# Kernel tuning notes

Hardware: AMD Instinct MI355X
Metric: run time of the kernel (lower is better)

Reference implementation:

```python
import jax, jax.numpy as jnp
import numpy as np

N, C, EMB_ROWS = 524288, 128, 32
SLOPE = 0.2  # leaky_relu negative slope


def setup_inputs() -> dict:
    key = jax.random.key(0)
    k1, k2, k3, k4, k5 = jax.random.split(key, 5)
    x = jax.random.normal(k1, (N, C), jnp.float32)
    perm = jax.random.permutation(k2, N)  # fixed stand-in for torch.randperm
    depth = jax.random.normal(k3, (EMB_ROWS, 128), jnp.float32)  # Embedding(32,128), N(0,1) init
    fan_in = 2 * C * 2
    bound = 1.0 / np.sqrt(fan_in)
    W = jax.random.uniform(k4, (C, 2 * C, 2), jnp.float32, -bound, bound)  # Conv1d weight (O,I,K)
    b = jax.random.uniform(k5, (C,), jnp.float32, -bound, bound)
    return {"x": x, "depth": depth, "W": W, "b": b, "perm": perm}


def reference(x, depth, W, b, perm):
    c = W.shape[0]
    x = x[perm]                      # random shuffle of rows
    x = x.T.reshape(1, c, -1)        # [1, C, N]
    i = 0
    # Python while over STATIC shapes -> unrolled at trace time (~log2(N) steps)
    while x.shape[-1] > 1:
        L = x.shape[-1]
        e = jnp.broadcast_to(depth[i].reshape(1, 128, 1), (1, 128, L))
        x = jnp.concatenate([x, e], axis=1)   # [1, 2C, L]
        x = jax.lax.conv_general_dilated(
            x, W, window_strides=(1,), padding="VALID",
            dimension_numbers=("NCH", "OIH", "NCH"))  # [1, C, L-1]
        x = x + b.reshape(1, -1, 1)
        x = jnp.where(x >= 0, x, SLOPE * x)   # leaky_relu(0.2)
        if x.shape[-1] == 1:
            break
        # MaxPool1d(2,2): floor(L/2), drops trailing element for odd L
        x = jax.lax.reduce_window(
            x, -jnp.inf, jax.lax.max,
            window_dimensions=(1, 1, 2), window_strides=(1, 1, 2),
            padding="VALID")
        i += 1
    return x.reshape(c, 1).T  # [1, C]
```

## Files before the change

kernel.cpp:

```cpp
#include <hip/hip_runtime.h>
#include <hip/hip_bf16.h>


typedef __bf16 v8bf __attribute__((ext_vector_type(8)));
typedef float v16f __attribute__((ext_vector_type(16)));

__device__ __forceinline__ ushort f2bf(float f) {
    __hip_bfloat16 h = __float2bfloat16(f);
    return *reinterpret_cast<ushort*>(&h);
}
__device__ __forceinline__ unsigned pack2(float lo, float hi) {
    return (unsigned)f2bf(lo) | ((unsigned)f2bf(hi) << 16);
}
__device__ __forceinline__ float leaky(float y) { return (y >= 0.f) ? y : 0.2f * y; }

#define ZACC {0.f,0.f,0.f,0.f,0.f,0.f,0.f,0.f,0.f,0.f,0.f,0.f,0.f,0.f,0.f,0.f}

__global__ void bias_kernel(const float* __restrict__ W, const float* __restrict__ b,
                            const float* __restrict__ depth, float* __restrict__ Bst) {
    int i = blockIdx.x, o = threadIdx.x;
    const float* Wo = W + (size_t)o * 512 + 256;
    const float* di = depth + (size_t)i * 128;
    float s = b[o];
#pragma unroll 8
    for (int c = 0; c < 128; ++c) s += di[c] * (Wo[2 * c] + Wo[2 * c + 1]);
    Bst[i * 128 + o] = s;
}

__global__ void repack_kernel(const float* __restrict__ W, ushort* __restrict__ A) {
    int o = blockIdx.x, c = threadIdx.x;
    float v = (c < 128) ? W[(size_t)o * 512 + 2 * c] : W[(size_t)o * 512 + 2 * (c - 128) + 1];
    A[o * 256 + c] = f2bf(v);
}

#define WAVE_SETUP()                                                          \
    const int tid = threadIdx.x;                                              \
    const int lane = tid & 63;                                                \
    const int w = tid >> 6;                                                   \
    const int n31 = lane & 31;                                                \
    const int h = lane >> 5;                                                  \
    v8bf af[16];                                                              \
    {                                                                         \
        const ushort* Arow = A + (size_t)(w * 32 + n31) * 256 + h * 8;        \
        _Pragma("unroll")                                                     \
        for (int s = 0; s < 16; ++s) af[s] = *(const v8bf*)&Arow[s * 16];     \
    }

#define LOAD_BIAS(dst_, Bs)                                                   \
    float dst_[16];                                                           \
    _Pragma("unroll")                                                         \
    for (int r = 0; r < 16; ++r)                                              \
        dst_[r] = (Bs)[w * 32 + (r & 3) + 8 * (r >> 2) + 4 * h];

#define MFMA_TILE_LDS(buf, r0_, r1_, acc)                                     \
    {                                                                         \
        const ushort* sp0 = (buf) + (r0_) * 128;                              \
        const ushort* sp1 = (buf) + (r1_) * 128;                              \
        const int mm0 = (r0_) & 15, mm1 = (r1_) & 15;                         \
        _Pragma("unroll")                                                     \
        for (int s = 0; s < 8; ++s)                                           \
            acc = __builtin_amdgcn_mfma_f32_32x32x16_bf16(                    \
                af[s], *(const v8bf*)&sp0[((2 * s + h) ^ mm0) * 8], acc, 0, 0, 0); \
        _Pragma("unroll")                                                     \
        for (int s = 0; s < 8; ++s)                                           \
            acc = __builtin_amdgcn_mfma_f32_32x32x16_bf16(                    \
                af[8 + s], *(const v8bf*)&sp1[((2 * s + h) ^ mm1) * 8], acc, 0, 0, 0); \
    }

__global__ __launch_bounds__(256)
void pair_fused(const ushort* __restrict__ Xin,
                const float* __restrict__ x0,
                const int* __restrict__ perm,
                const ushort* __restrict__ A,
                const float* __restrict__ Bst2,
                ushort* __restrict__ Y,
                int Lin, int Lp2, int stage0) {
    __shared__ __align__(16) ushort xin[132 * 128];
    __shared__ __align__(16) ushort mid[65 * 128];
    __shared__ int prow[132];

    const int U = blockIdx.x * 32;
    const int t0 = U * 4;

    if (stage0) {
        for (int r = threadIdx.x; r < 132; r += 256)
            prow[r] = perm[min(t0 + r, Lin - 1)];
        __syncthreads();
    }
    for (int idx = threadIdx.x; idx < 132 * 16; idx += 256) {
        int row = idx >> 4, ck = idx & 15;
        int t = min(t0 + row, Lin - 1);
        int dst = row * 128 + ((ck ^ (row & 15)) * 8);
        if (stage0) {
            const float* s = x0 + (size_t)prow[row] * 128 + ck * 8;
            float4 a = *(const float4*)s;
            float4 bq = *(const float4*)(s + 4);
            uint4 v;
            v.x = pack2(a.x, a.y);  v.y = pack2(a.z, a.w);
            v.z = pack2(bq.x, bq.y); v.w = pack2(bq.z, bq.w);
            *(uint4*)&xin[dst] = v;
        } else {
            *(uint4*)&xin[dst] = *(const uint4*)&Xin[(size_t)t * 128 + ck * 8];
        }
    }
    __syncthreads();

    WAVE_SETUP();

    {
        LOAD_BIAS(bias_r, Bst2);
#pragma unroll
        for (int ti = 0; ti < 5; ++ti) {
            const int p = 32 * ti + n31;
            const int r0 = min(p, 131), r1 = min(p + 1, 131);
            v16f acc = ZACC;
            MFMA_TILE_LDS(xin, r0, r1, acc);
            const int u1 = 16 * ti + (n31 >> 1);
            const bool act = !(lane & 1) && (u1 < 65);
#pragma unroll
            for (int q = 0; q < 4; ++q) {
                float pv[4];
#pragma unroll
                for (int j = 0; j < 4; ++j) {
                    float y = leaky(acc[4 * q + j] + bias_r[4 * q + j]);
                    float y2 = __shfl_xor(y, 1, 64);
                    pv[j] = fmaxf(y, y2);
                }
                if (act) {
                    uint2 v;
                    v.x = pack2(pv[0], pv[1]);
                    v.y = pack2(pv[2], pv[3]);
                    *(uint2*)&mid[u1 * 128 + (((4 * w + q) ^ (u1 & 15)) * 8) + 4 * h] = v;
                }
            }
        }
    }
    __syncthreads();

    {
        LOAD_BIAS(bias_r, Bst2 + 128);
#pragma unroll
        for (int ti = 0; ti < 2; ++ti) {
            const int p = 32 * ti + n31;
            v16f acc = ZACC;
            MFMA_TILE_LDS(mid, p, p + 1, acc);
            const int u2 = U + 16 * ti + (n31 >> 1);
            const bool act = !(lane & 1) && (u2 < Lp2);
#pragma unroll
            for (int q = 0; q < 4; ++q) {
                float pv[4];
#pragma unroll
                for (int j = 0; j < 4; ++j) {
                    float y = leaky(acc[4 * q + j] + bias_r[4 * q + j]);
                    float y2 = __shfl_xor(y, 1, 64);
                    pv[j] = fmaxf(y, y2);
                }
                if (act) {
                    uint2 v;
                    v.x = pack2(pv[0], pv[1]);
                    v.y = pack2(pv[2], pv[3]);
                    *(uint2*)&Y[(size_t)u2 * 128 + w * 32 + 8 * q + 4 * h] = v;
                }
            }
        }
    }
}

__global__ __launch_bounds__(256)
void tail_fused(const ushort* __restrict__ Xg, const ushort* __restrict__ A,
                const float* __restrict__ BstAll, float* __restrict__ out) {
    extern __shared__ __align__(16) ushort tbuf[];
    ushort* buf0 = tbuf;
    ushort* buf1 = tbuf + 255 * 128;

    WAVE_SETUP();

    int Lin = 511;
    for (int st = 0; st < 8; ++st) {
        const int Lp = (Lin - 1) >> 1;
        LOAD_BIAS(bias_r, BstAll + (size_t)(10 + st) * 128);
        ushort* dst = (st & 1) ? buf1 : buf0;
        const ushort* src = (st & 1) ? buf0 : buf1;
        const int ntiles = (Lin - 1 + 31) >> 5;
        for (int ti = 0; ti < ntiles; ++ti) {
            const int t = ti * 32 + n31;
            const int r0 = min(t, Lin - 1), r1 = min(t + 1, Lin - 1);
            v16f acc = ZACC;
            if (st == 0) {
                const ushort* p0 = Xg + (size_t)r0 * 128 + h * 8;
                const ushort* p1 = Xg + (size_t)r1 * 128 + h * 8;
#pragma unroll
                for (int s = 0; s < 8; ++s)
                    acc = __builtin_amdgcn_mfma_f32_32x32x16_bf16(
                        af[s], *(const v8bf*)&p0[s * 16], acc, 0, 0, 0);
#pragma unroll
                for (int s = 0; s < 8; ++s)
                    acc = __builtin_amdgcn_mfma_f32_32x32x16_bf16(
                        af[8 + s], *(const v8bf*)&p1[s * 16], acc, 0, 0, 0);
            } else {
                MFMA_TILE_LDS(src, r0, r1, acc);
            }
            const int u = t >> 1;
            const bool act = !(lane & 1) && (u < Lp);
#pragma unroll
            for (int q = 0; q < 4; ++q) {
                float pv[4];
#pragma unroll
                for (int j = 0; j < 4; ++j) {
                    float y = leaky(acc[4 * q + j] + bias_r[4 * q + j]);
                    float y2 = __shfl_xor(y, 1, 64);
                    pv[j] = fmaxf(y, y2);
                }
                if (act) {
                    if (st < 7) {
                        uint2 v;
                        v.x = pack2(pv[0], pv[1]);
                        v.y = pack2(pv[2], pv[3]);
                        *(uint2*)&dst[u * 128 + (((4 * w + q) ^ (u & 15)) * 8) + 4 * h] = v;
                    } else {
                        float4 o = {pv[0], pv[1], pv[2], pv[3]};
                        *(float4*)&out[w * 32 + 8 * q + 4 * h] = o;
                    }
                }
            }
        }
        __syncthreads();
        Lin = Lp;
    }
}

extern "C" void kernel_launch(void* const* d_in, const int* in_sizes, int n_in,
                              void* d_out, int out_size, void* d_ws, size_t ws_size,
                              hipStream_t stream) {
    const float* x     = (const float*)d_in[0];
    const float* depth = (const float*)d_in[1];
    const float* W     = (const float*)d_in[2];
    const float* b     = (const float*)d_in[3];
    const int*   perm  = (const int*)d_in[4];
    float* out = (float*)d_out;

    char* ws = (char*)d_ws;
    float*  Bst = (float*)ws;
    ushort* A   = (ushort*)(ws + 16384);
    ushort* R0  = (ushort*)(ws + 16384 + 65536);
    ushort* R1  = (ushort*)(ws + 16384 + 65536 + (size_t)131071 * 256);

    bias_kernel<<<18, 128, 0, stream>>>(W, b, depth, Bst);
    repack_kernel<<<128, 256, 0, stream>>>(W, A);

    pair_fused<<<4096, 256, 0, stream>>>(nullptr, x, perm, A, Bst, R0,
                                         524288, 131071, 1);
    pair_fused<<<1024, 256, 0, stream>>>(R0, nullptr, nullptr, A, Bst + 2 * 128, R1,
                                         131071, 32767, 0);
    pair_fused<<<256, 256, 0, stream>>>(R1, nullptr, nullptr, A, Bst + 4 * 128, R0,
                                        32767, 8191, 0);
    pair_fused<<<64, 256, 0, stream>>>(R0, nullptr, nullptr, A, Bst + 6 * 128, R1,
                                       8191, 2047, 0);
    pair_fused<<<16, 256, 0, stream>>>(R1, nullptr, nullptr, A, Bst + 8 * 128, R0,
                                       2047, 511, 0);
    tail_fused<<<1, 256, (255 + 127) * 128 * 2, stream>>>(R0, A, Bst, out);
}
```

Baseline: 555.9 us.

## Fuse all stages into one persistent cooperative kernel with grid syncs

Replaces the chain of seven launches (prep, five pair stages, tail) with a single cooperative persistent kernel that loops blocks over the tiles of each stage and separates stages with grid.sync, keeping the weight fragments in registers across stages. The tail now ping-pongs through global scratch instead of LDS, and the perm lookup is done per element instead of staged in shared memory. This is meant to remove launch gaps and tail-effect idle time between the small late stages. In exchange it adds grid-barrier cost and occupancy limits from cooperative launch, and the tail's global-memory round trips may be slower than LDS.

Measured after the change: 889.6 us. 60.0% more time.

```diff
diff --git a/kernel.cpp b/kernel.cpp
--- a/kernel.cpp
+++ b/kernel.cpp
@@ -1,5 +1,8 @@
 #include <hip/hip_runtime.h>
 #include <hip/hip_bf16.h>
+#include <hip/hip_cooperative_groups.h>
+
+namespace cg = cooperative_groups;
 
 
 typedef __bf16 v8bf __attribute__((ext_vector_type(8)));
@@ -16,83 +19,33 @@
 
 #define ZACC {0.f,0.f,0.f,0.f,0.f,0.f,0.f,0.f,0.f,0.f,0.f,0.f,0.f,0.f,0.f,0.f}
 
-__global__ void bias_kernel(const float* __restrict__ W, const float* __restrict__ b,
-                            const float* __restrict__ depth, float* __restrict__ Bst) {
-    int i = blockIdx.x, o = threadIdx.x;
-    const float* Wo = W + (size_t)o * 512 + 256;
-    const float* di = depth + (size_t)i * 128;
-    float s = b[o];
-#pragma unroll 8
-    for (int c = 0; c < 128; ++c) s += di[c] * (Wo[2 * c] + Wo[2 * c + 1]);
-    Bst[i * 128 + o] = s;
-}
-
-__global__ void repack_kernel(const float* __restrict__ W, ushort* __restrict__ A) {
-    int o = blockIdx.x, c = threadIdx.x;
-    float v = (c < 128) ? W[(size_t)o * 512 + 2 * c] : W[(size_t)o * 512 + 2 * (c - 128) + 1];
-    A[o * 256 + c] = f2bf(v);
-}
-
-#define WAVE_SETUP()                                                          \
-    const int tid = threadIdx.x;                                              \
-    const int lane = tid & 63;                                                \
-    const int w = tid >> 6;                                                   \
-    const int n31 = lane & 31;                                                \
-    const int h = lane >> 5;                                                  \
-    v8bf af[16];                                                              \
-    {                                                                         \
-        const ushort* Arow = A + (size_t)(w * 32 + n31) * 256 + h * 8;        \
-        _Pragma("unroll")                                                     \
-        for (int s = 0; s < 16; ++s) af[s] = *(const v8bf*)&Arow[s * 16];     \
-    }
-
-#define LOAD_BIAS(dst_, Bs)                                                   \
-    float dst_[16];                                                           \
-    _Pragma("unroll")                                                         \
-    for (int r = 0; r < 16; ++r)                                              \
-        dst_[r] = (Bs)[w * 32 + (r & 3) + 8 * (r >> 2) + 4 * h];
-
-#define MFMA_TILE_LDS(buf, r0_, r1_, acc)                                     \
-    {                                                                         \
-        const ushort* sp0 = (buf) + (r0_) * 128;                              \
-        const ushort* sp1 = (buf) + (r1_) * 128;                              \
-        const int mm0 = (r0_) & 15, mm1 = (r1_) & 15;                         \
-        _Pragma("unroll")                                                     \
-        for (int s = 0; s < 8; ++s)                                           \
-            acc = __builtin_amdgcn_mfma_f32_32x32x16_bf16(                    \
-                af[s], *(const v8bf*)&sp0[((2 * s + h) ^ mm0) * 8], acc, 0, 0, 0); \
-        _Pragma("unroll")                                                     \
-        for (int s = 0; s < 8; ++s)                                           \
-            acc = __builtin_amdgcn_mfma_f32_32x32x16_bf16(                    \
-                af[8 + s], *(const v8bf*)&sp1[((2 * s + h) ^ mm1) * 8], acc, 0, 0, 0); \
-    }
-
-__global__ __launch_bounds__(256)
-void pair_fused(const ushort* __restrict__ Xin,
-                const float* __restrict__ x0,
-                const int* __restrict__ perm,
-                const ushort* __restrict__ A,
-                const float* __restrict__ Bst2,
-                ushort* __restrict__ Y,
-                int Lin, int Lp2, int stage0) {
-    __shared__ __align__(16) ushort xin[132 * 128];
-    __shared__ __align__(16) ushort mid[65 * 128];
-    __shared__ int prow[132];
-
-    const int U = blockIdx.x * 32;
+__device__ __forceinline__ void load_af(const ushort* __restrict__ A, v8bf* af) {
+    const int lane = threadIdx.x & 63;
+    const int w = threadIdx.x >> 6;
+    const ushort* Arow = A + (size_t)(w * 32 + (lane & 31)) * 256 + (lane >> 5) * 8;
+#pragma unroll
+    for (int s = 0; s < 16; ++s) af[s] = *(const v8bf*)&Arow[s * 16];
+}
+
+__device__ void do_pair(int U, const ushort* __restrict__ Xin,
+                        const float* __restrict__ x0, const int* __restrict__ perm,
+                        const v8bf* af, const float* __restrict__ Bst2,
+                        ushort* __restrict__ Y, int Lin, int Lp2, int stage0,
+                        ushort* xin, ushort* mid) {
+    const int tid = threadIdx.x;
+    const int lane = tid & 63;
+    const int w = tid >> 6;
+    const int n31 = lane & 31;
+    const int h = lane >> 5;
     const int t0 = U * 4;
 
-    if (stage0) {
-        for (int r = threadIdx.x; r < 132; r += 256)
-            prow[r] = perm[min(t0 + r, Lin - 1)];
-        __syncthreads();
-    }
-    for (int idx = threadIdx.x; idx < 132 * 16; idx += 256) {
+    for (int idx = tid; idx < 132 * 16; idx += 256) {
         int row = idx >> 4, ck = idx & 15;
         int t = min(t0 + row, Lin - 1);
         int dst = row * 128 + ((ck ^ (row & 15)) * 8);
         if (stage0) {
-            const float* s = x0 + (size_t)prow[row] * 128 + ck * 8;
+            int pr = perm[t];
+            const float* s = x0 + (size_t)pr * 128 + ck * 8;
             float4 a = *(const float4*)s;
             float4 bq = *(const float4*)(s + 4);
             uint4 v;
@@ -105,16 +58,27 @@
     }
     __syncthreads();
 
-    WAVE_SETUP();
-
     {
-        LOAD_BIAS(bias_r, Bst2);
+        float bias_r[16];
+#pragma unroll
+        for (int r = 0; r < 16; ++r)
+            bias_r[r] = Bst2[w * 32 + (r & 3) + 8 * (r >> 2) + 4 * h];
 #pragma unroll
         for (int ti = 0; ti < 5; ++ti) {
             const int p = 32 * ti + n31;
             const int r0 = min(p, 131), r1 = min(p + 1, 131);
+            const ushort* sp0 = xin + r0 * 128;
+            const ushort* sp1 = xin + r1 * 128;
+            const int m0 = r0 & 15, m1 = r1 & 15;
             v16f acc = ZACC;
-            MFMA_TILE_LDS(xin, r0, r1, acc);
+#pragma unroll
+            for (int s = 0; s < 8; ++s)
+                acc = __builtin_amdgcn_mfma_f32_32x32x16_bf16(
+                    af[s], *(const v8bf*)&sp0[((2 * s + h) ^ m0) * 8], acc, 0, 0, 0);
+#pragma unroll
+            for (int s = 0; s < 8; ++s)
+                acc = __builtin_amdgcn_mfma_f32_32x32x16_bf16(
+                    af[8 + s], *(const v8bf*)&sp1[((2 * s + h) ^ m1) * 8], acc, 0, 0, 0);
             const int u1 = 16 * ti + (n31 >> 1);
             const bool act = !(lane & 1) && (u1 < 65);
 #pragma unroll
@@ -138,12 +102,25 @@
     __syncthreads();
 
     {
-        LOAD_BIAS(bias_r, Bst2 + 128);
+        float bias_r[16];
+#pragma unroll
+        for (int r = 0; r < 16; ++r)
+            bias_r[r] = Bst2[128 + w * 32 + (r & 3) + 8 * (r >> 2) + 4 * h];
 #pragma unroll
         for (int ti = 0; ti < 2; ++ti) {
             const int p = 32 * ti + n31;
+            const ushort* sp0 = mid + p * 128;
+            const ushort* sp1 = mid + (p + 1) * 128;
+            const int m0 = p & 15, m1 = (p + 1) & 15;
             v16f acc = ZACC;
-            MFMA_TILE_LDS(mid, p, p + 1, acc);
+#pragma unroll
+            for (int s = 0; s < 8; ++s)
+                acc = __builtin_amdgcn_mfma_f32_32x32x16_bf16(
+                    af[s], *(const v8bf*)&sp0[((2 * s + h) ^ m0) * 8], acc, 0, 0, 0);
+#pragma unroll
+            for (int s = 0; s < 8; ++s)
+                acc = __builtin_amdgcn_mfma_f32_32x32x16_bf16(
+                    af[8 + s], *(const v8bf*)&sp1[((2 * s + h) ^ m1) * 8], acc, 0, 0, 0);
             const int u2 = U + 16 * ti + (n31 >> 1);
             const bool act = !(lane & 1) && (u2 < Lp2);
 #pragma unroll
@@ -166,40 +143,39 @@
     }
 }
 
-__global__ __launch_bounds__(256)
-void tail_fused(const ushort* __restrict__ Xg, const ushort* __restrict__ A,
-                const float* __restrict__ BstAll, float* __restrict__ out) {
-    extern __shared__ __align__(16) ushort tbuf[];
-    ushort* buf0 = tbuf;
-    ushort* buf1 = tbuf + 255 * 128;
-
-    WAVE_SETUP();
+__device__ void do_tail(const ushort* __restrict__ Xg, ushort* __restrict__ T0,
+                        ushort* __restrict__ T1, const v8bf* af,
+                        const float* __restrict__ BstAll, float* __restrict__ out) {
+    const int tid = threadIdx.x;
+    const int lane = tid & 63;
+    const int w = tid >> 6;
+    const int n31 = lane & 31;
+    const int h = lane >> 5;
 
     int Lin = 511;
+    const ushort* src = Xg;
     for (int st = 0; st < 8; ++st) {
         const int Lp = (Lin - 1) >> 1;
-        LOAD_BIAS(bias_r, BstAll + (size_t)(10 + st) * 128);
-        ushort* dst = (st & 1) ? buf1 : buf0;
-        const ushort* src = (st & 1) ? buf0 : buf1;
+        float bias_r[16];
+#pragma unroll
+        for (int r = 0; r < 16; ++r)
+            bias_r[r] = BstAll[(10 + st) * 128 + w * 32 + (r & 3) + 8 * (r >> 2) + 4 * h];
+        ushort* dst = (st & 1) ? T1 : T0;
         const int ntiles = (Lin - 1 + 31) >> 5;
         for (int ti = 0; ti < ntiles; ++ti) {
             const int t = ti * 32 + n31;
             const int r0 = min(t, Lin - 1), r1 = min(t + 1, Lin - 1);
+            const ushort* p0 = src + (size_t)r0 * 128 + h * 8;
+            const ushort* p1 = src + (size_t)r1 * 128 + h * 8;
             v16f acc = ZACC;
-            if (st == 0) {
-                const ushort* p0 = Xg + (size_t)r0 * 128 + h * 8;
-                const ushort* p1 = Xg + (size_t)r1 * 128 + h * 8;
-#pragma unroll
-                for (int s = 0; s < 8; ++s)
-                    acc = __builtin_amdgcn_mfma_f32_32x32x16_bf16(
-                        af[s], *(const v8bf*)&p0[s * 16], acc, 0, 0, 0);
-#pragma unroll
-                for (int s = 0; s < 8; ++s)
-                    acc = __builtin_amdgcn_mfma_f32_32x32x16_bf16(
-                        af[8 + s], *(const v8bf*)&p1[s * 16], acc, 0, 0, 0);
-            } else {
-                MFMA_TILE_LDS(src, r0, r1, acc);
-            }
+#pragma unroll
+            for (int s = 0; s < 8; ++s)
+                acc = __builtin_amdgcn_mfma_f32_32x32x16_bf16(
+                    af[s], *(const v8bf*)&p0[s * 16], acc, 0, 0, 0);
+#pragma unroll
+            for (int s = 0; s < 8; ++s)
+                acc = __builtin_amdgcn_mfma_f32_32x32x16_bf16(
+                    af[8 + s], *(const v8bf*)&p1[s * 16], acc, 0, 0, 0);
             const int u = t >> 1;
             const bool act = !(lane & 1) && (u < Lp);
 #pragma unroll
@@ -216,7 +192,7 @@
                         uint2 v;
                         v.x = pack2(pv[0], pv[1]);
                         v.y = pack2(pv[2], pv[3]);
-                        *(uint2*)&dst[u * 128 + (((4 * w + q) ^ (u & 15)) * 8) + 4 * h] = v;
+                        *(uint2*)&dst[u * 128 + w * 32 + 8 * q + 4 * h] = v;
                     } else {
                         float4 o = {pv[0], pv[1], pv[2], pv[3]};
                         *(float4*)&out[w * 32 + 8 * q + 4 * h] = o;
@@ -224,9 +200,95 @@
                 }
             }
         }
+        __threadfence();
         __syncthreads();
+        src = dst;
         Lin = Lp;
     }
+}
+
+__device__ void do_prep(int gt, const float* __restrict__ Wf, const float* __restrict__ bv,
+                        const float* __restrict__ depth, float* __restrict__ Bst,
+                        ushort* __restrict__ A) {
+    if (gt < 2304) {
+        int i = gt >> 7, o = gt & 127;
+        const float* Wo = Wf + (size_t)o * 512 + 256;
+        const float* di = depth + (size_t)i * 128;
+        float s = bv[o];
+#pragma unroll 8
+        for (int c = 0; c < 128; ++c) s += di[c] * (Wo[2 * c] + Wo[2 * c + 1]);
+        Bst[i * 128 + o] = s;
+    }
+    int gr = gt - 2304;
+    if (gr >= 0 && gr < 32768) {
+        int o = gr >> 8, c = gr & 255;
+        float v = (c < 128) ? Wf[(size_t)o * 512 + 2 * c]
+                            : Wf[(size_t)o * 512 + 2 * (c - 128) + 1];
+        A[o * 256 + c] = f2bf(v);
+    }
+}
+
+__global__ __launch_bounds__(256, 2)
+void mono_kernel(const float* __restrict__ x0, const float* __restrict__ depth,
+                 const float* __restrict__ Wf, const float* __restrict__ bv,
+                 const int* __restrict__ perm, float* __restrict__ Bst,
+                 ushort* __restrict__ A, ushort* __restrict__ R0,
+                 ushort* __restrict__ R1, float* __restrict__ out) {
+    __shared__ __align__(16) ushort xin[132 * 128];
+    __shared__ __align__(16) ushort mid[65 * 128];
+    cg::grid_group grid = cg::this_grid();
+    const int bid = blockIdx.x, nb = gridDim.x;
+
+    do_prep(bid * 256 + threadIdx.x, Wf, bv, depth, Bst, A);
+    grid.sync();
+
+    v8bf af[16];
+    load_af(A, af);
+
+    for (int g = bid; g < 4096; g += nb)
+        do_pair(g * 32, nullptr, x0, perm, af, Bst, R0, 524288, 131071, 1, xin, mid);
+    grid.sync();
+    for (int g = bid; g < 1024; g += nb)
+        do_pair(g * 32, R0, nullptr, nullptr, af, Bst + 2 * 128, R1, 131071, 32767, 0, xin, mid);
+    grid.sync();
+    for (int g = bid; g < 256; g += nb)
+        do_pair(g * 32, R1, nullptr, nullptr, af, Bst + 4 * 128, R0, 32767, 8191, 0, xin, mid);
+    grid.sync();
+    for (int g = bid; g < 64; g += nb)
+        do_pair(g * 32, R0, nullptr, nullptr, af, Bst + 6 * 128, R1, 8191, 2047, 0, xin, mid);
+    grid.sync();
+    for (int g = bid; g < 16; g += nb)
+        do_pair(g * 32, R1, nullptr, nullptr, af, Bst + 8 * 128, R0, 2047, 511, 0, xin, mid);
+    grid.sync();
+
+    if (bid == 0) do_tail(R0, R1, R1 + 255 * 128, af, Bst, out);
+}
+
+__global__ void prep_kernel(const float* __restrict__ Wf, const float* __restrict__ bv,
+                            const float* __restrict__ depth, float* __restrict__ Bst,
+                            ushort* __restrict__ A) {
+    do_prep(blockIdx.x * 256 + threadIdx.x, Wf, bv, depth, Bst, A);
+}
+
+__global__ __launch_bounds__(256)
+void pair_kernel(const ushort* __restrict__ Xin, const float* __restrict__ x0,
+                 const int* __restrict__ perm, const ushort* __restrict__ A,
+                 const float* __restrict__ Bst2, ushort* __restrict__ Y,
+                 int Lin, int Lp2, int stage0) {
+    __shared__ __align__(16) ushort xin[132 * 128];
+    __shared__ __align__(16) ushort mid[65 * 128];
+    v8bf af[16];
+    load_af(A, af);
+    do_pair(blockIdx.x * 32, Xin, x0, perm, af, Bst2, Y, Lin, Lp2, stage0, xin, mid);
+}
+
+__global__ __launch_bounds__(256)
+void tail_kernel(const ushort* __restrict__ Xg, ushort* __restrict__ T0,
+                 ushort* __restrict__ T1, const ushort* __restrict__ A,
+                 const float* __restrict__ BstAll, float* __restrict__ out) {
+    v8bf af[16];
+    load_af(A, af);
+    do_tail(Xg, T0, T1, af, BstAll, out);
 }
 
 extern "C" void kernel_launch(void* const* d_in, const int* in_sizes, int n_in,
@@ -245,18 +307,33 @@
     ushort* R0  = (ushort*)(ws + 16384 + 65536);
     ushort* R1  = (ushort*)(ws + 16384 + 65536 + (size_t)131071 * 256);
 
-    bias_kernel<<<18, 128, 0, stream>>>(W, b, depth, Bst);
-    repack_kernel<<<128, 256, 0, stream>>>(W, A);
-
-    pair_fused<<<4096, 256, 0, stream>>>(nullptr, x, perm, A, Bst, R0,
-                                         524288, 131071, 1);
-    pair_fused<<<1024, 256, 0, stream>>>(R0, nullptr, nullptr, A, Bst + 2 * 128, R1,
-                                         131071, 32767, 0);
-    pair_fused<<<256, 256, 0, stream>>>(R1, nullptr, nullptr, A, Bst + 4 * 128, R0,
-                                        32767, 8191, 0);
-    pair_fused<<<64, 256, 0, stream>>>(R0, nullptr, nullptr, A, Bst + 6 * 128, R1,
-                                       8191, 2047, 0);
-    pair_fused<<<16, 256, 0, stream>>>(R1, nullptr, nullptr, A, Bst + 8 * 128, R0,
-                                       2047, 511, 0);
-    tail_fused<<<1, 256, (255 + 127) * 128 * 2, stream>>>(R0, A, Bst, out);
-}
+    int maxb = 0;
+    hipError_t qe = hipOccupancyMaxActiveBlocksPerMultiprocessor(&maxb, mono_kernel, 256, 0);
+    if (qe != hipSuccess || maxb < 1) maxb = 0;
+    int nblk = maxb * 256;
+    if (nblk > 1024) nblk = 1024;
+
+    hipError_t rc = hipErrorUnknown;
+    if (nblk >= 256) {
+        const float* xa = x; const float* da = depth; const float* Wa = W;
+        const float* ba = b; const int* pa = perm;
+        float* Ba = Bst; ushort* Aa = A; ushort* R0a = R0; ushort* R1a = R1;
+        float* oa = out;
+        void* args[] = {&xa, &da, &Wa, &ba, &pa, &Ba, &Aa, &R0a, &R1a, &oa};
+        rc = hipLaunchCooperativeKernel(mono_kernel, dim3(nblk), dim3(256), args, 0, stream);
+    }
+    if (rc != hipSuccess) {
+        prep_kernel<<<137, 256, 0, stream>>>(W, b, depth, Bst, A);
+        pair_kernel<<<4096, 256, 0, stream>>>(nullptr, x, perm, A, Bst, R0,
+                                              524288, 131071, 1);
+        pair_kernel<<<1024, 256, 0, stream>>>(R0, nullptr, nullptr, A, Bst + 2 * 128, R1,
+                                              131071, 32767, 0);
+        pair_kernel<<<256, 256, 0, stream>>>(R1, nullptr, nullptr, A, Bst + 4 * 128, R0,
+                                             32767, 8191, 0);
+        pair_kernel<<<64, 256, 0, stream>>>(R0, nullptr, nullptr, A, Bst + 6 * 128, R1,
+                                            8191, 2047, 0);
+        pair_kernel<<<16, 256, 0, stream>>>(R1, nullptr, nullptr, A, Bst + 8 * 128, R0,
+                                            2047, 511, 0);
+        tail_kernel<<<1, 256, 0, stream>>>(R0, R1, R1 + 255 * 128, A, Bst, out);
+    }
+}
```
